# Optimization experiments

Hardware: AMD Instinct MI355X
Metric: run time of the kernel (lower is better)

The kernel has to match this reference:

```python
import jax, jax.numpy as jnp
import numpy as np

N = 50000
E = 800000
NEG_SLOPE = 0.2  # PyG GATConv default


def gat_conv(x, src, dst, W, att_src, att_dst, bias, heads, out_ch, concat):
    # x: [N, F_in]; W: [F_in, heads*out_ch]; att_*: [heads, out_ch]; bias: [heads*out_ch] or [out_ch]
    h = (x @ W).reshape(N, heads, out_ch)                       # [N, H, C]
    a_src = jnp.sum(h * att_src, axis=-1)                       # [N, H]
    a_dst = jnp.sum(h * att_dst, axis=-1)                       # [N, H]
    e = jax.nn.leaky_relu(a_src[src] + a_dst[dst], NEG_SLOPE)   # [E', H]
    # numerically stable scatter-softmax over incoming edges of each dst node
    e_max = jax.ops.segment_max(e, dst, num_segments=N)         # [N, H]
    ex = jnp.exp(e - e_max[dst])                                # [E', H]
    denom = jax.ops.segment_sum(ex, dst, num_segments=N)        # [N, H]
    alpha = ex / denom[dst]                                     # [E', H]
    msg = h[src] * alpha[:, :, None]                            # [E', H, C]
    out = jax.ops.segment_sum(msg, dst, num_segments=N)         # [N, H, C]
    out = out.reshape(N, heads * out_ch) if concat else out.mean(axis=1)
    return out + bias


def setup_inputs() -> dict:
    key = jax.random.key(0)
    ks = jax.random.split(key, 16)
    s = 0.05
    x = jax.random.normal(ks[0], (N, 128), dtype=jnp.float32)
    edge_index = jax.random.randint(ks[1], (2, E), 0, N, dtype=jnp.int64)
    H, C = 8, 64
    return {
        "x": x,
        "edge_index": edge_index,
        "W0": jax.random.normal(ks[2], (128, H * C), dtype=jnp.float32) * s,
        "as0": jax.random.normal(ks[3], (H, C), dtype=jnp.float32) * s,
        "ad0": jax.random.normal(ks[4], (H, C), dtype=jnp.float32) * s,
        "b0": jnp.zeros((H * C,), dtype=jnp.float32),
        "W1": jax.random.normal(ks[5], (H * C, H * C), dtype=jnp.float32) * s,
        "as1": jax.random.normal(ks[6], (H, C), dtype=jnp.float32) * s,
        "ad1": jax.random.normal(ks[7], (H, C), dtype=jnp.float32) * s,
        "b1": jnp.zeros((H * C,), dtype=jnp.float32),
        "W2": jax.random.normal(ks[8], (H * C, 40), dtype=jnp.float32) * s,
        "as2": jax.random.normal(ks[9], (1, 40), dtype=jnp.float32) * s,
        "ad2": jax.random.normal(ks[10], (1, 40), dtype=jnp.float32) * s,
        "b2": jnp.zeros((40,), dtype=jnp.float32),
    }


def reference(x, edge_index, W0, as0, ad0, b0, W1, as1, ad1, b1, W2, as2, ad2, b2):
    # add self-loops (PyG GATConv default add_self_loops=True)
    loop = jnp.arange(N, dtype=edge_index.dtype)
    src = jnp.concatenate([edge_index[0], loop])
    dst = jnp.concatenate([edge_index[1], loop])
    h = gat_conv(x, src, dst, W0, as0, ad0, b0, heads=8, out_ch=64, concat=True)
    h = jax.nn.relu(h)  # dropout is identity at inference
    h = gat_conv(h, src, dst, W1, as1, ad1, b1, heads=8, out_ch=64, concat=True)
    h = jax.nn.relu(h)
    h = gat_conv(h, src, dst, W2, as2, ad2, b2, heads=1, out_ch=40, concat=False)
    return jax.nn.log_softmax(h, axis=1)
```

## Files before the change

### kernel.cpp

```cpp
#include <hip/hip_runtime.h>
#include <hip/hip_bf16.h>
#include <hip/hip_fp16.h>
#include <math.h>

#define N_NODES 50000
#define N_EDGES 800000
#define TOT_EDGES (N_EDGES + N_NODES)
#define NEG_SLOPE 0.2f
#define M_PAD 50048
#define N_CHUNKS ((N_NODES + 1023) / 1024)

typedef __attribute__((ext_vector_type(8))) short bf16x8;
typedef __attribute__((ext_vector_type(4))) float f32x4;
typedef __attribute__((ext_vector_type(8))) unsigned short u16x8;

__device__ __forceinline__ unsigned short f2bf(float f){
  union { float f; unsigned u; } x; x.f = f;
  unsigned r = x.u + 0x7FFF + ((x.u >> 16) & 1);
  return (unsigned short)(r >> 16);
}
__device__ __forceinline__ float bf2f(unsigned short h){
  union { unsigned u; float f; } x; x.u = ((unsigned)h) << 16;
  return x.f;
}
__device__ __forceinline__ void gl_lds16(const void* g, void* l){
  __builtin_amdgcn_global_load_lds(
    (const __attribute__((address_space(1))) unsigned int*)g,
    (__attribute__((address_space(3))) unsigned int*)l, 16, 0, 0);
}


__global__ void hist_kernel(const int* __restrict__ ei, int* __restrict__ counts){
  int e = blockIdx.x*256 + threadIdx.x;
  if (e >= TOT_EDGES) return;
  int d = (e < N_EDGES) ? ei[N_EDGES + e] : (e - N_EDGES);
  atomicAdd(&counts[d], 1);
}

__global__ void scan1_kernel(const int* __restrict__ counts, int* __restrict__ partial,
                             int* __restrict__ chunksum){
  __shared__ int sm[1024];
  int t = threadIdx.x;
  int idx = blockIdx.x*1024 + t;
  int v = (idx < N_NODES) ? counts[idx] : 0;
  sm[t] = v;
  __syncthreads();
  for (int off = 1; off < 1024; off <<= 1){
    int u = (t >= off) ? sm[t-off] : 0;
    __syncthreads();
    sm[t] += u;
    __syncthreads();
  }
  if (idx < N_NODES) partial[idx] = sm[t];
  if (t == 1023) chunksum[blockIdx.x] = sm[1023];
}

__global__ void scan2_kernel(const int* __restrict__ chunksum, int* __restrict__ carry){
  if (threadIdx.x == 0){
    int c = 0;
    for (int i = 0; i < N_CHUNKS; ++i){ carry[i] = c; c += chunksum[i]; }
  }
}

__global__ void scan3_kernel(const int* __restrict__ partial, const int* __restrict__ counts,
                             const int* __restrict__ carry, int* __restrict__ offsets,
                             int* __restrict__ cursor){
  int idx = blockIdx.x*256 + threadIdx.x;
  if (idx >= N_NODES) return;
  int inc = partial[idx] + carry[idx >> 10];
  offsets[idx+1] = inc;
  cursor[idx] = inc - counts[idx];
  if (idx == 0) offsets[0] = 0;
}

__global__ void scatter_kernel(const int* __restrict__ ei, int* __restrict__ cursor,
                               int* __restrict__ ssrc){
  int e = blockIdx.x*256 + threadIdx.x;
  if (e >= TOT_EDGES) return;
  int s, d;
  if (e < N_EDGES){ s = ei[e]; d = ei[N_EDGES+e]; } else { s = e - N_EDGES; d = s; }
  int pos = atomicAdd(&cursor[d], 1);
  ssrc[pos] = s;
}


__global__ void convert_BT(const float* __restrict__ B, unsigned short* __restrict__ BTh,
                           unsigned short* __restrict__ BTl, int K, int N){
  int id = blockIdx.x*256 + threadIdx.x;
  if (id >= K*N) return;
  int n = id / K, k = id - n*K;
  float v = B[(size_t)k*N + n];
  unsigned short h = f2bf(v);
  unsigned short l = f2bf(v - bf2f(h));
  BTh[id] = h; BTl[id] = l;
}

__global__ void convert_BT2(const float* __restrict__ B, unsigned short* __restrict__ BTh,
                            unsigned short* __restrict__ BTl){
  int id = blockIdx.x*256 + threadIdx.x;
  if (id >= 128*512) return;
  int n = id >> 9, k = id & 511;
  float v = (n < 40) ? B[(size_t)k*40 + n] : 0.f;
  unsigned short h = f2bf(v);
  unsigned short l = f2bf(v - bf2f(h));
  BTh[id] = h; BTl[id] = l;
}

__global__ void split_x(const float* __restrict__ X, unsigned short* __restrict__ Xh,
                        unsigned short* __restrict__ Xl){
  int id = blockIdx.x*256 + threadIdx.x;
  if (id >= M_PAD*128) return;
  int row = id >> 7;
  float v = (row < N_NODES) ? X[(size_t)row*128 + (id & 127)] : 0.f;
  unsigned short h = f2bf(v);
  unsigned short l = f2bf(v - bf2f(h));
  Xh[id] = h; Xl[id] = l;
}


__global__ __launch_bounds__(256, 2) void mfma_gemm(
    const unsigned short* __restrict__ Ah_g, const unsigned short* __restrict__ Al_g,
    const unsigned short* __restrict__ BTh, const unsigned short* __restrict__ BTl,
    float* __restrict__ C, unsigned short* __restrict__ FbS,
    const float* __restrict__ att_s, const float* __restrict__ att_d,
    float* __restrict__ asrc, float* __restrict__ adst,
    int M, int K, int Nc)
{
  __shared__ unsigned short sAh[128*32];
  __shared__ unsigned short sAl[128*32];
  __shared__ unsigned short sBh[128*32];
  __shared__ unsigned short sBl[128*32];

  const int tid = threadIdx.x;
  const int lane = tid & 63;
  const int wid = tid >> 6;
  const int wr = wid >> 1, wc = wid & 1;
  const int bm = blockIdx.y * 128, bn = blockIdx.x * 128;
  const int lr = lane & 15, kg = lane >> 4;

  size_t agoff[2], bgoff[2];
  #pragma unroll
  for (int i = 0; i < 2; ++i){
    int o = tid + i*256;
    int row = o >> 2, ch = o & 3;
    int sc = ch ^ ((row >> 1) & 3);
    agoff[i] = (size_t)(bm + row)*K + sc*8;
    bgoff[i] = (size_t)(bn + row)*K + sc*8;
  }
  int aoff[4], boff[4];
  #pragma unroll
  for (int i = 0; i < 4; ++i){
    int row = wr*64 + i*16 + lr;
    aoff[i] = row*32 + (kg ^ ((row >> 1) & 3))*8;
    int col = wc*64 + i*16 + lr;
    boff[i] = col*32 + (kg ^ ((col >> 1) & 3))*8;
  }

  auto stage = [&](int k0){
    #pragma unroll
    for (int i = 0; i < 2; ++i){
      gl_lds16(Ah_g + agoff[i] + k0, &sAh[(tid + i*256)*8]);
      gl_lds16(Al_g + agoff[i] + k0, &sAl[(tid + i*256)*8]);
      gl_lds16(BTh + bgoff[i] + k0, &sBh[(tid + i*256)*8]);
      gl_lds16(BTl + bgoff[i] + k0, &sBl[(tid + i*256)*8]);
    }
  };

  f32x4 acc[4][4];
  #pragma unroll
  for (int i = 0; i < 4; ++i)
    #pragma unroll
    for (int j = 0; j < 4; ++j)
      acc[i][j] = (f32x4){0.f, 0.f, 0.f, 0.f};

  stage(0);
  __syncthreads();
  int k0 = 0;
  while (true){
    bf16x8 ah[4], al[4], bh[4], bl[4];
    #pragma unroll
    for (int i = 0; i < 4; ++i){
      ah[i] = *(const bf16x8*)&sAh[aoff[i]];
      al[i] = *(const bf16x8*)&sAl[aoff[i]];
      bh[i] = *(const bf16x8*)&sBh[boff[i]];
      bl[i] = *(const bf16x8*)&sBl[boff[i]];
    }
    #pragma unroll
    for (int i = 0; i < 4; ++i)
      #pragma unroll
      for (int j = 0; j < 4; ++j){
        acc[i][j] = __builtin_amdgcn_mfma_f32_16x16x32_bf16(ah[i], bh[j], acc[i][j], 0, 0, 0);
        acc[i][j] = __builtin_amdgcn_mfma_f32_16x16x32_bf16(al[i], bh[j], acc[i][j], 0, 0, 0);
        acc[i][j] = __builtin_amdgcn_mfma_f32_16x16x32_bf16(ah[i], bl[j], acc[i][j], 0, 0, 0);
      }
    int kn = k0 + 32;
    if (kn >= K) break;
    __syncthreads();
    stage(kn);
    __syncthreads();
    k0 = kn;
  }

  if (att_s){
    int head = (bn >> 6) + wc;
    float ws_[4], wd_[4];
    #pragma unroll
    for (int j = 0; j < 4; ++j){
      ws_[j] = att_s[head*64 + j*16 + lr];
      wd_[j] = att_d[head*64 + j*16 + lr];
    }
    #pragma unroll
    for (int i = 0; i < 4; ++i){
      #pragma unroll
      for (int r = 0; r < 4; ++r){
        float vs = 0.f, vd = 0.f;
        #pragma unroll
        for (int j = 0; j < 4; ++j){
          vs += acc[i][j][r] * ws_[j];
          vd += acc[i][j][r] * wd_[j];
        }
        #pragma unroll
        for (int m = 1; m < 16; m <<= 1){
          vs += __shfl_xor(vs, m);
          vd += __shfl_xor(vd, m);
        }
        int gm = bm + wr*64 + i*16 + kg*4 + r;
        if ((lane & 15) == 0 && gm < M){
          asrc[gm*8 + head] = vs;
          adst[gm*8 + head] = vd;
        }
      }
    }
  }

  #pragma unroll
  for (int i = 0; i < 4; ++i){
    int gm0 = bm + wr*64 + i*16 + kg*4;
    #pragma unroll
    for (int j = 0; j < 4; ++j){
      int gn = bn + wc*64 + j*16 + lr;
      int sl = gn >> 5, cc = gn & 31;
      #pragma unroll
      for (int r = 0; r < 4; ++r){
        int gm = gm0 + r;
        if (gm < M){
          if (C && gn < Nc) C[(size_t)gm*Nc + gn] = acc[i][j][r];
          if (FbS) FbS[(size_t)sl*(M_PAD*32) + (size_t)gm*32 + cc] = f2bf(acc[i][j][r]);
        }
      }
    }
  }
}


__global__ __launch_bounds__(256) void softmax_stats(const int* __restrict__ offsets,
    const int* __restrict__ ssrc, const float* __restrict__ asrc,
    const float* __restrict__ adst, unsigned* __restrict__ EA){
  int w = threadIdx.x >> 6;
  int lane = threadIdx.x & 63;
  int d = blockIdx.x*4 + w;
  if (d >= N_NODES) return;
  int h = lane & 7, grp = lane >> 3;
  int beg = offsets[d], end = offsets[d+1];
  float ad = adst[d*8+h];
  float pm = -1e30f;
  for (int i = beg+grp; i < end; i += 8){
    int s = ssrc[i];
    float e = asrc[s*8+h] + ad;
    e = (e > 0.f) ? e : NEG_SLOPE*e;
    pm = fmaxf(pm, e);
  }
  pm = fmaxf(pm, __shfl_xor(pm, 8));
  pm = fmaxf(pm, __shfl_xor(pm, 16));
  pm = fmaxf(pm, __shfl_xor(pm, 32));
  float ps = 0.f;
  for (int i = beg+grp; i < end; i += 8){
    int s = ssrc[i];
    float e = asrc[s*8+h] + ad;
    e = (e > 0.f) ? e : NEG_SLOPE*e;
    ps += __expf(e - pm);
  }
  ps += __shfl_xor(ps, 8);
  ps += __shfl_xor(ps, 16);
  ps += __shfl_xor(ps, 32);
  float iv = 1.f / ps;
  unsigned* Eh = EA + (size_t)h * TOT_EDGES;
  for (int i = beg+grp; i < end; i += 8){
    int s = ssrc[i];
    float e = asrc[s*8+h] + ad;
    e = (e > 0.f) ? e : NEG_SLOPE*e;
    float al = __expf(e - pm) * iv;
    union { __half hh; unsigned short u; } cv; cv.hh = __float2half(al);
    unsigned pk = (unsigned)s | ((unsigned)cv.u << 16);
    __builtin_nontemporal_store(pk, &Eh[i]);
  }
}


__global__ __launch_bounds__(256) void spmm_kernel(const unsigned short* __restrict__ FbS,
    const int* __restrict__ offsets, const unsigned* __restrict__ EA,
    const float* __restrict__ bias, unsigned short* __restrict__ Fh,
    unsigned short* __restrict__ Fl, int do_relu){
  __shared__ unsigned sEA[1024];
  int bid = blockIdx.x;
  int half = (bid >= 25000) ? 1 : 0;
  int r = bid - half*25000;
  int slice = (r & 7) + half*8;
  int chunk = r >> 3;
  int lane = threadIdx.x & 63;
  int wid = threadIdx.x >> 6;
  int dsub = lane >> 4;
  int slot = (lane >> 2) & 3;
  int ch = lane & 3;
  int dbase = chunk*16;
  int d = dbase + wid*4 + dsub;
  int h = slice >> 1;
  const unsigned short* Ft = FbS + (size_t)slice * (M_PAD*32);
  const unsigned* Eh = EA + (size_t)h * TOT_EDGES;
  int beg0 = offsets[dbase];
  int cnt = min(offsets[dbase+16] - beg0, 1024);
  for (int i = threadIdx.x; i < cnt; i += 256)
    sEA[i] = __builtin_nontemporal_load(&Eh[beg0 + i]);
  __syncthreads();
  int beg = offsets[d], end = offsets[d+1];
  float a0=0.f,a1=0.f,a2=0.f,a3=0.f,a4=0.f,a5=0.f,a6=0.f,a7=0.f;
  #pragma unroll 2
  for (int i = beg + slot; i < end; i += 4){
    int idx = i - beg0;
    unsigned ea = (idx < cnt) ? sEA[idx] : __builtin_nontemporal_load(&Eh[i]);
    int s = ea & 0xFFFF;
    union { unsigned short u; __half hh; } dv; dv.u = (unsigned short)(ea >> 16);
    float al = __half2float(dv.hh);
    uint4 v = *(const uint4*)&Ft[(size_t)s*32 + ch*8];
    union { unsigned q; float f; } lo, hi;
    lo.q = v.x << 16; hi.q = v.x & 0xffff0000u; a0 += al*lo.f; a1 += al*hi.f;
    lo.q = v.y << 16; hi.q = v.y & 0xffff0000u; a2 += al*lo.f; a3 += al*hi.f;
    lo.q = v.z << 16; hi.q = v.z & 0xffff0000u; a4 += al*lo.f; a5 += al*hi.f;
    lo.q = v.w << 16; hi.q = v.w & 0xffff0000u; a6 += al*lo.f; a7 += al*hi.f;
  }
  a0 += __shfl_xor(a0, 4); a0 += __shfl_xor(a0, 8);
  a1 += __shfl_xor(a1, 4); a1 += __shfl_xor(a1, 8);
  a2 += __shfl_xor(a2, 4); a2 += __shfl_xor(a2, 8);
  a3 += __shfl_xor(a3, 4); a3 += __shfl_xor(a3, 8);
  a4 += __shfl_xor(a4, 4); a4 += __shfl_xor(a4, 8);
  a5 += __shfl_xor(a5, 4); a5 += __shfl_xor(a5, 8);
  a6 += __shfl_xor(a6, 4); a6 += __shfl_xor(a6, 8);
  a7 += __shfl_xor(a7, 4); a7 += __shfl_xor(a7, 8);
  if (slot == 0){
    int c = slice*32 + ch*8;
    float4 b0v = *(const float4*)&bias[c];
    float4 b1v = *(const float4*)&bias[c+4];
    float oo[8];
    oo[0]=a0+b0v.x; oo[1]=a1+b0v.y; oo[2]=a2+b0v.z; oo[3]=a3+b0v.w;
    oo[4]=a4+b1v.x; oo[5]=a5+b1v.y; oo[6]=a6+b1v.z; oo[7]=a7+b1v.w;
    u16x8 vh, vl;
    #pragma unroll
    for (int q = 0; q < 8; ++q){
      float v = oo[q];
      if (do_relu) v = fmaxf(v, 0.f);
      unsigned short hb = f2bf(v);
      vh[q] = hb;
      vl[q] = f2bf(v - bf2f(hb));
    }
    size_t base = (size_t)d*512 + c;
    *(u16x8*)&Fh[base] = vh;
    *(u16x8*)&Fl[base] = vl;
  }
}


__global__ void attn_coef2_kernel(const float* __restrict__ H2v, const float* __restrict__ as2,
                                  const float* __restrict__ ad2,
                                  float* __restrict__ asrc, float* __restrict__ adst){
  int gid = blockIdx.x*256 + threadIdx.x;
  int node = gid >> 6;
  int lane = threadIdx.x & 63;
  if (node >= N_NODES) return;
  float v = 0.f, ws = 0.f, wd = 0.f;
  if (lane < 40){ v = H2v[(size_t)node*40 + lane]; ws = as2[lane]; wd = ad2[lane]; }
  float vs = v*ws, vd = v*wd;
  #pragma unroll
  for (int off = 32; off > 0; off >>= 1){
    vs += __shfl_down(vs, off);
    vd += __shfl_down(vd, off);
  }
  if (lane == 0){ asrc[node] = vs; adst[node] = vd; }
}

__global__ __launch_bounds__(64) void aggregate2_kernel(const float* __restrict__ H2v,
    const int* __restrict__ offsets, const int* __restrict__ ssrc,
    const float* __restrict__ asrc, const float* __restrict__ adst,
    const float* __restrict__ bias, float* __restrict__ OUT){
  int d = blockIdx.x;
  int lane = threadIdx.x;
  int beg = offsets[d], end = offsets[d+1];
  int deg = end - beg;
  float ad = adst[d];
  float pm = -1e30f;
  for (int i = lane; i < deg; i += 64){
    int s = ssrc[beg+i];
    float e = asrc[s] + ad; e = (e>0.f)?e:NEG_SLOPE*e;
    pm = fmaxf(pm, e);
  }
  #pragma unroll
  for (int off = 32; off > 0; off >>= 1) pm = fmaxf(pm, __shfl_xor(pm, off));
  float ps = 0.f;
  for (int i = lane; i < deg; i += 64){
    int s = ssrc[beg+i];
    float e = asrc[s] + ad; e=(e>0.f)?e:NEG_SLOPE*e;
    ps += __expf(e - pm);
  }
  #pragma unroll
  for (int off = 32; off > 0; off >>= 1) ps += __shfl_xor(ps, off);
  float inv = 1.f/ps;
  __shared__ float alS[64];
  __shared__ int sS[64];
  float acc = 0.f;
  for (int i0 = 0; i0 < deg; i0 += 64){
    int nch = min(64, deg - i0);
    if (lane < nch){
      int s = ssrc[beg+i0+lane];
      float e = asrc[s]+ad; e=(e>0.f)?e:NEG_SLOPE*e;
      alS[lane] = __expf(e-pm)*inv;
      sS[lane] = s;
    }
    __syncthreads();
    for (int i = 0; i < nch; ++i){
      if (lane < 40) acc += alS[i] * H2v[(size_t)sS[i]*40 + lane];
    }
    __syncthreads();
  }
  float logit = (lane<40) ? (acc + bias[lane]) : -1e30f;
  float mm = logit;
  #pragma unroll
  for (int off = 32; off > 0; off >>= 1) mm = fmaxf(mm, __shfl_xor(mm, off));
  float ex = (lane<40) ? __expf(logit-mm) : 0.f;
  float ss = ex;
  #pragma unroll
  for (int off = 32; off > 0; off >>= 1) ss += __shfl_xor(ss, off);
  if (lane < 40) OUT[(size_t)d*40 + lane] = logit - mm - logf(ss);
}


extern "C" void kernel_launch(void* const* d_in, const int* in_sizes, int n_in,
                              void* d_out, int out_size, void* d_ws, size_t ws_size,
                              hipStream_t stream){
  const float* x   = (const float*)d_in[0];
  const int*   ei  = (const int*)d_in[1];
  const float* W0  = (const float*)d_in[2];
  const float* as0 = (const float*)d_in[3];
  const float* ad0 = (const float*)d_in[4];
  const float* b0  = (const float*)d_in[5];
  const float* W1  = (const float*)d_in[6];
  const float* as1 = (const float*)d_in[7];
  const float* ad1 = (const float*)d_in[8];
  const float* b1  = (const float*)d_in[9];
  const float* W2  = (const float*)d_in[10];
  const float* as2 = (const float*)d_in[11];
  const float* ad2 = (const float*)d_in[12];
  const float* b2  = (const float*)d_in[13];
  float* out = (float*)d_out;

  char* p = (char*)d_ws;
  auto alloc = [&](size_t bytes)->void*{
    void* r = (void*)p; p += (bytes + 255) & ~(size_t)255; return r;
  };
  unsigned short* F1h = (unsigned short*)alloc((size_t)M_PAD*512*2);
  unsigned short* F1l = (unsigned short*)alloc((size_t)M_PAD*512*2);
  unsigned short* FbS = (unsigned short*)alloc((size_t)M_PAD*512*2);
  unsigned short* Xh  = (unsigned short*)alloc((size_t)M_PAD*128*2);
  unsigned short* Xl  = (unsigned short*)alloc((size_t)M_PAD*128*2);
  float* ASRC  = (float*)alloc((size_t)N_NODES*8*4);
  float* ADST  = (float*)alloc((size_t)N_NODES*8*4);
  unsigned* EA = (unsigned*)alloc((size_t)8*TOT_EDGES*4);
  float* H2v   = (float*)alloc((size_t)N_NODES*40*4);
  float* ASRC2 = (float*)alloc((size_t)N_NODES*4);
  float* ADST2 = (float*)alloc((size_t)N_NODES*4);
  int* counts  = (int*)alloc((size_t)N_NODES*4);
  int* offsets = (int*)alloc((size_t)(N_NODES+1)*4);
  int* cursor  = (int*)alloc((size_t)N_NODES*4);
  int* ssrc    = (int*)alloc((size_t)TOT_EDGES*4);
  int* partial = (int*)alloc((size_t)N_NODES*4);
  int* chunksum= (int*)alloc(64*4);
  int* carry   = (int*)alloc(64*4);
  unsigned short* BTh  = (unsigned short*)alloc((size_t)512*512*2);
  unsigned short* BTl  = (unsigned short*)alloc((size_t)512*512*2);
  unsigned short* BT2h = (unsigned short*)alloc((size_t)128*512*2);
  unsigned short* BT2l = (unsigned short*)alloc((size_t)128*512*2);

  hipMemsetAsync(F1h + (size_t)N_NODES*512, 0, (size_t)(M_PAD-N_NODES)*512*2, stream);
  hipMemsetAsync(F1l + (size_t)N_NODES*512, 0, (size_t)(M_PAD-N_NODES)*512*2, stream);

  hipMemsetAsync(counts, 0, (size_t)N_NODES*4, stream);
  hist_kernel<<<(TOT_EDGES+255)/256, 256, 0, stream>>>(ei, counts);
  scan1_kernel<<<N_CHUNKS, 1024, 0, stream>>>(counts, partial, chunksum);
  scan2_kernel<<<1, 64, 0, stream>>>(chunksum, carry);
  scan3_kernel<<<(N_NODES+255)/256, 256, 0, stream>>>(partial, counts, carry, offsets, cursor);
  scatter_kernel<<<(TOT_EDGES+255)/256, 256, 0, stream>>>(ei, cursor, ssrc);

  int mt = M_PAD / 128;
  int spmm_blocks = 2 * 8 * 3125;

  split_x<<<(M_PAD*128+255)/256, 256, 0, stream>>>(x, Xh, Xl);
  convert_BT<<<(128*512+255)/256, 256, 0, stream>>>(W0, BTh, BTl, 128, 512);
  mfma_gemm<<<dim3(4, mt), 256, 0, stream>>>(Xh, Xl, BTh, BTl, nullptr, FbS,
                                             as0, ad0, ASRC, ADST, N_NODES, 128, 512);
  softmax_stats<<<(N_NODES+3)/4, 256, 0, stream>>>(offsets, ssrc, ASRC, ADST, EA);
  spmm_kernel<<<spmm_blocks, 256, 0, stream>>>(FbS, offsets, EA, b0, F1h, F1l, 1);

  convert_BT<<<(512*512+255)/256, 256, 0, stream>>>(W1, BTh, BTl, 512, 512);
  mfma_gemm<<<dim3(4, mt), 256, 0, stream>>>(F1h, F1l, BTh, BTl, nullptr, FbS,
                                             as1, ad1, ASRC, ADST, N_NODES, 512, 512);
  softmax_stats<<<(N_NODES+3)/4, 256, 0, stream>>>(offsets, ssrc, ASRC, ADST, EA);
  spmm_kernel<<<spmm_blocks, 256, 0, stream>>>(FbS, offsets, EA, b1, F1h, F1l, 1);

  convert_BT2<<<(128*512+255)/256, 256, 0, stream>>>(W2, BT2h, BT2l);
  mfma_gemm<<<dim3(1, mt), 256, 0, stream>>>(F1h, F1l, BT2h, BT2l, H2v, nullptr,
                                             nullptr, nullptr, nullptr, nullptr, N_NODES, 512, 40);
  attn_coef2_kernel<<<(N_NODES*64+255)/256, 256, 0, stream>>>(H2v, as2, ad2, ASRC2, ADST2);
  aggregate2_kernel<<<N_NODES, 64, 0, stream>>>(H2v, offsets, ssrc, ASRC2, ADST2, b2, out);
}
```

Baseline: 767.6 us.

## Switch GEMM to fp16 two-term split, online softmax stats, drop spmm LDS staging

The split-bf16 GEMM becomes fp16 MFMA. A is still split into high and low halves, but B is a single fp16 copy, so each tile needs two MFMAs instead of three and one fewer LDS buffer. The softmax stats kernel now computes max and sum in one online pass instead of two passes over the edges. The spmm kernel drops its LDS prefetch of edge data and loads it directly, and features are stored as fp16 rather than bf16. fp16 has a narrower range than bf16 and B loses its low-order correction, which risks accuracy or overflow.

```diff
diff --git a/kernel.cpp b/kernel.cpp
--- a/kernel.cpp
+++ b/kernel.cpp
@@ -10,18 +10,15 @@
 #define M_PAD 50048
 #define N_CHUNKS ((N_NODES + 1023) / 1024)
 
-typedef __attribute__((ext_vector_type(8))) short bf16x8;
+typedef __attribute__((ext_vector_type(8))) _Float16 f16x8;
 typedef __attribute__((ext_vector_type(4))) float f32x4;
 typedef __attribute__((ext_vector_type(8))) unsigned short u16x8;
 
-__device__ __forceinline__ unsigned short f2bf(float f){
-  union { float f; unsigned u; } x; x.f = f;
-  unsigned r = x.u + 0x7FFF + ((x.u >> 16) & 1);
-  return (unsigned short)(r >> 16);
-}
-__device__ __forceinline__ float bf2f(unsigned short h){
-  union { unsigned u; float f; } x; x.u = ((unsigned)h) << 16;
-  return x.f;
+__device__ __forceinline__ unsigned short f2h(float f){
+  union { _Float16 h; unsigned short u; } c; c.h = (_Float16)f; return c.u;
+}
+__device__ __forceinline__ float h2f(unsigned short u){
+  union { unsigned short u; _Float16 h; } c; c.u = u; return (float)c.h;
 }
 __device__ __forceinline__ void gl_lds16(const void* g, void* l){
   __builtin_amdgcn_global_load_lds(
@@ -84,26 +81,19 @@
 }
 
 
-__global__ void convert_BT(const float* __restrict__ B, unsigned short* __restrict__ BTh,
-                           unsigned short* __restrict__ BTl, int K, int N){
+__global__ void convert_BT(const float* __restrict__ B, unsigned short* __restrict__ BT,
+                           int K, int N){
   int id = blockIdx.x*256 + threadIdx.x;
   if (id >= K*N) return;
   int n = id / K, k = id - n*K;
-  float v = B[(size_t)k*N + n];
-  unsigned short h = f2bf(v);
-  unsigned short l = f2bf(v - bf2f(h));
-  BTh[id] = h; BTl[id] = l;
-}
-
-__global__ void convert_BT2(const float* __restrict__ B, unsigned short* __restrict__ BTh,
-                            unsigned short* __restrict__ BTl){
+  BT[id] = f2h(B[(size_t)k*N + n]);
+}
+
+__global__ void convert_BT2(const float* __restrict__ B, unsigned short* __restrict__ BT){
   int id = blockIdx.x*256 + threadIdx.x;
   if (id >= 128*512) return;
   int n = id >> 9, k = id & 511;
-  float v = (n < 40) ? B[(size_t)k*40 + n] : 0.f;
-  unsigned short h = f2bf(v);
-  unsigned short l = f2bf(v - bf2f(h));
-  BTh[id] = h; BTl[id] = l;
+  BT[id] = f2h((n < 40) ? B[(size_t)k*40 + n] : 0.f);
 }
 
 __global__ void split_x(const float* __restrict__ X, unsigned short* __restrict__ Xh,
@@ -112,15 +102,15 @@
   if (id >= M_PAD*128) return;
   int row = id >> 7;
   float v = (row < N_NODES) ? X[(size_t)row*128 + (id & 127)] : 0.f;
-  unsigned short h = f2bf(v);
-  unsigned short l = f2bf(v - bf2f(h));
-  Xh[id] = h; Xl[id] = l;
+  unsigned short h = f2h(v);
+  Xh[id] = h;
+  Xl[id] = f2h(v - h2f(h));
 }
 
 
 __global__ __launch_bounds__(256, 2) void mfma_gemm(
     const unsigned short* __restrict__ Ah_g, const unsigned short* __restrict__ Al_g,
-    const unsigned short* __restrict__ BTh, const unsigned short* __restrict__ BTl,
+    const unsigned short* __restrict__ BT,
     float* __restrict__ C, unsigned short* __restrict__ FbS,
     const float* __restrict__ att_s, const float* __restrict__ att_d,
     float* __restrict__ asrc, float* __restrict__ adst,
@@ -128,8 +118,7 @@
 {
   __shared__ unsigned short sAh[128*32];
   __shared__ unsigned short sAl[128*32];
-  __shared__ unsigned short sBh[128*32];
-  __shared__ unsigned short sBl[128*32];
+  __shared__ unsigned short sB[128*32];
 
   const int tid = threadIdx.x;
   const int lane = tid & 63;
@@ -161,8 +150,7 @@
     for (int i = 0; i < 2; ++i){
       gl_lds16(Ah_g + agoff[i] + k0, &sAh[(tid + i*256)*8]);
       gl_lds16(Al_g + agoff[i] + k0, &sAl[(tid + i*256)*8]);
-      gl_lds16(BTh + bgoff[i] + k0, &sBh[(tid + i*256)*8]);
-      gl_lds16(BTl + bgoff[i] + k0, &sBl[(tid + i*256)*8]);
+      gl_lds16(BT + bgoff[i] + k0, &sB[(tid + i*256)*8]);
     }
   };
 
@@ -177,21 +165,19 @@
   __syncthreads();
   int k0 = 0;
   while (true){
-    bf16x8 ah[4], al[4], bh[4], bl[4];
+    f16x8 ah[4], al[4], b[4];
     #pragma unroll
     for (int i = 0; i < 4; ++i){
-      ah[i] = *(const bf16x8*)&sAh[aoff[i]];
-      al[i] = *(const bf16x8*)&sAl[aoff[i]];
-      bh[i] = *(const bf16x8*)&sBh[boff[i]];
-      bl[i] = *(const bf16x8*)&sBl[boff[i]];
+      ah[i] = *(const f16x8*)&sAh[aoff[i]];
+      al[i] = *(const f16x8*)&sAl[aoff[i]];
+      b[i]  = *(const f16x8*)&sB[boff[i]];
     }
     #pragma unroll
     for (int i = 0; i < 4; ++i)
       #pragma unroll
       for (int j = 0; j < 4; ++j){
-        acc[i][j] = __builtin_amdgcn_mfma_f32_16x16x32_bf16(ah[i], bh[j], acc[i][j], 0, 0, 0);
-        acc[i][j] = __builtin_amdgcn_mfma_f32_16x16x32_bf16(al[i], bh[j], acc[i][j], 0, 0, 0);
-        acc[i][j] = __builtin_amdgcn_mfma_f32_16x16x32_bf16(ah[i], bl[j], acc[i][j], 0, 0, 0);
+        acc[i][j] = __builtin_amdgcn_mfma_f32_16x16x32_f16(ah[i], b[j], acc[i][j], 0, 0, 0);
+        acc[i][j] = __builtin_amdgcn_mfma_f32_16x16x32_f16(al[i], b[j], acc[i][j], 0, 0, 0);
       }
     int kn = k0 + 32;
     if (kn >= K) break;
@@ -245,7 +231,7 @@
         int gm = gm0 + r;
         if (gm < M){
           if (C && gn < Nc) C[(size_t)gm*Nc + gn] = acc[i][j][r];
-          if (FbS) FbS[(size_t)sl*(M_PAD*32) + (size_t)gm*32 + cc] = f2bf(acc[i][j][r]);
+          if (FbS) FbS[(size_t)sl*(M_PAD*32) + (size_t)gm*32 + cc] = f2h(acc[i][j][r]);
         }
       }
     }
@@ -263,35 +249,30 @@
   int h = lane & 7, grp = lane >> 3;
   int beg = offsets[d], end = offsets[d+1];
   float ad = adst[d*8+h];
-  float pm = -1e30f;
+  float m = -1e30f, s = 0.f;
   for (int i = beg+grp; i < end; i += 8){
-    int s = ssrc[i];
-    float e = asrc[s*8+h] + ad;
+    int sv = ssrc[i];
+    float e = asrc[sv*8+h] + ad;
     e = (e > 0.f) ? e : NEG_SLOPE*e;
-    pm = fmaxf(pm, e);
-  }
-  pm = fmaxf(pm, __shfl_xor(pm, 8));
-  pm = fmaxf(pm, __shfl_xor(pm, 16));
-  pm = fmaxf(pm, __shfl_xor(pm, 32));
-  float ps = 0.f;
-  for (int i = beg+grp; i < end; i += 8){
-    int s = ssrc[i];
-    float e = asrc[s*8+h] + ad;
-    e = (e > 0.f) ? e : NEG_SLOPE*e;
-    ps += __expf(e - pm);
-  }
-  ps += __shfl_xor(ps, 8);
-  ps += __shfl_xor(ps, 16);
-  ps += __shfl_xor(ps, 32);
-  float iv = 1.f / ps;
+    if (e > m){ s = s*__expf(m - e) + 1.f; m = e; }
+    else s += __expf(e - m);
+  }
+  #pragma unroll
+  for (int k = 8; k < 64; k <<= 1){
+    float mo = __shfl_xor(m, k);
+    float so = __shfl_xor(s, k);
+    float M = fmaxf(m, mo);
+    s = s*__expf(m - M) + so*__expf(mo - M);
+    m = M;
+  }
+  float iv = 1.f / s;
   unsigned* Eh = EA + (size_t)h * TOT_EDGES;
   for (int i = beg+grp; i < end; i += 8){
-    int s = ssrc[i];
-    float e = asrc[s*8+h] + ad;
+    int sv = ssrc[i];
+    float e = asrc[sv*8+h] + ad;
     e = (e > 0.f) ? e : NEG_SLOPE*e;
-    float al = __expf(e - pm) * iv;
-    union { __half hh; unsigned short u; } cv; cv.hh = __float2half(al);
-    unsigned pk = (unsigned)s | ((unsigned)cv.u << 16);
+    float al = __expf(e - m) * iv;
+    unsigned pk = (unsigned)sv | ((unsigned)f2h(al) << 16);
     __builtin_nontemporal_store(pk, &Eh[i]);
   }
 }
@@ -301,7 +282,6 @@
     const int* __restrict__ offsets, const unsigned* __restrict__ EA,
     const float* __restrict__ bias, unsigned short* __restrict__ Fh,
     unsigned short* __restrict__ Fl, int do_relu){
-  __shared__ unsigned sEA[1024];
   int bid = blockIdx.x;
   int half = (bid >= 25000) ? 1 : 0;
   int r = bid - half*25000;
@@ -312,31 +292,27 @@
   int dsub = lane >> 4;
   int slot = (lane >> 2) & 3;
   int ch = lane & 3;
-  int dbase = chunk*16;
-  int d = dbase + wid*4 + dsub;
+  int d = chunk*16 + wid*4 + dsub;
   int h = slice >> 1;
   const unsigned short* Ft = FbS + (size_t)slice * (M_PAD*32);
   const unsigned* Eh = EA + (size_t)h * TOT_EDGES;
-  int beg0 = offsets[dbase];
-  int cnt = min(offsets[dbase+16] - beg0, 1024);
-  for (int i = threadIdx.x; i < cnt; i += 256)
-    sEA[i] = __builtin_nontemporal_load(&Eh[beg0 + i]);
-  __syncthreads();
-  int beg = offsets[d], end = offsets[d+1];
+  int2 oo = *(const int2*)&offsets[d];
+  int beg = oo.x, end = oo.y;
   float a0=0.f,a1=0.f,a2=0.f,a3=0.f,a4=0.f,a5=0.f,a6=0.f,a7=0.f;
   #pragma unroll 2
   for (int i = beg + slot; i < end; i += 4){
-    int idx = i - beg0;
-    unsigned ea = (idx < cnt) ? sEA[idx] : __builtin_nontemporal_load(&Eh[i]);
+    unsigned ea = __builtin_nontemporal_load(&Eh[i]);
     int s = ea & 0xFFFF;
-    union { unsigned short u; __half hh; } dv; dv.u = (unsigned short)(ea >> 16);
-    float al = __half2float(dv.hh);
-    uint4 v = *(const uint4*)&Ft[(size_t)s*32 + ch*8];
-    union { unsigned q; float f; } lo, hi;
-    lo.q = v.x << 16; hi.q = v.x & 0xffff0000u; a0 += al*lo.f; a1 += al*hi.f;
-    lo.q = v.y << 16; hi.q = v.y & 0xffff0000u; a2 += al*lo.f; a3 += al*hi.f;
-    lo.q = v.z << 16; hi.q = v.z & 0xffff0000u; a4 += al*lo.f; a5 += al*hi.f;
-    lo.q = v.w << 16; hi.q = v.w & 0xffff0000u; a6 += al*lo.f; a7 += al*hi.f;
+    float al = h2f((unsigned short)(ea >> 16));
+    f16x8 v = *(const f16x8*)&Ft[(size_t)s*32 + ch*8];
+    a0 += al * (float)v[0];
+    a1 += al * (float)v[1];
+    a2 += al * (float)v[2];
+    a3 += al * (float)v[3];
+    a4 += al * (float)v[4];
+    a5 += al * (float)v[5];
+    a6 += al * (float)v[6];
+    a7 += al * (float)v[7];
   }
   a0 += __shfl_xor(a0, 4); a0 += __shfl_xor(a0, 8);
   a1 += __shfl_xor(a1, 4); a1 += __shfl_xor(a1, 8);
@@ -350,17 +326,17 @@
     int c = slice*32 + ch*8;
     float4 b0v = *(const float4*)&bias[c];
     float4 b1v = *(const float4*)&bias[c+4];
-    float oo[8];
-    oo[0]=a0+b0v.x; oo[1]=a1+b0v.y; oo[2]=a2+b0v.z; oo[3]=a3+b0v.w;
-    oo[4]=a4+b1v.x; oo[5]=a5+b1v.y; oo[6]=a6+b1v.z; oo[7]=a7+b1v.w;
+    float oo_[8];
+    oo_[0]=a0+b0v.x; oo_[1]=a1+b0v.y; oo_[2]=a2+b0v.z; oo_[3]=a3+b0v.w;
+    oo_[4]=a4+b1v.x; oo_[5]=a5+b1v.y; oo_[6]=a6+b1v.z; oo_[7]=a7+b1v.w;
     u16x8 vh, vl;
     #pragma unroll
     for (int q = 0; q < 8; ++q){
-      float v = oo[q];
+      float v = oo_[q];
       if (do_relu) v = fmaxf(v, 0.f);
-      unsigned short hb = f2bf(v);
+      unsigned short hb = f2h(v);
       vh[q] = hb;
-      vl[q] = f2bf(v - bf2f(hb));
+      vl[q] = f2h(v - h2f(hb));
     }
     size_t base = (size_t)d*512 + c;
     *(u16x8*)&Fh[base] = vh;
@@ -483,10 +459,8 @@
   int* partial = (int*)alloc((size_t)N_NODES*4);
   int* chunksum= (int*)alloc(64*4);
   int* carry   = (int*)alloc(64*4);
-  unsigned short* BTh  = (unsigned short*)alloc((size_t)512*512*2);
-  unsigned short* BTl  = (unsigned short*)alloc((size_t)512*512*2);
-  unsigned short* BT2h = (unsigned short*)alloc((size_t)128*512*2);
-  unsigned short* BT2l = (unsigned short*)alloc((size_t)128*512*2);
+  unsigned short* BT  = (unsigned short*)alloc((size_t)512*512*2);
+  unsigned short* BT2 = (unsigned short*)alloc((size_t)128*512*2);
 
   hipMemsetAsync(F1h + (size_t)N_NODES*512, 0, (size_t)(M_PAD-N_NODES)*512*2, stream);
   hipMemsetAsync(F1l + (size_t)N_NODES*512, 0, (size_t)(M_PAD-N_NODES)*512*2, stream);
@@ -502,20 +476,20 @@
   int spmm_blocks = 2 * 8 * 3125;
 
   split_x<<<(M_PAD*128+255)/256, 256, 0, stream>>>(x, Xh, Xl);
-  convert_BT<<<(128*512+255)/256, 256, 0, stream>>>(W0, BTh, BTl, 128, 512);
-  mfma_gemm<<<dim3(4, mt), 256, 0, stream>>>(Xh, Xl, BTh, BTl, nullptr, FbS,
+  convert_BT<<<(128*512+255)/256, 256, 0, stream>>>(W0, BT, 128, 512);
+  mfma_gemm<<<dim3(4, mt), 256, 0, stream>>>(Xh, Xl, BT, nullptr, FbS,
                                              as0, ad0, ASRC, ADST, N_NODES, 128, 512);
   softmax_stats<<<(N_NODES+3)/4, 256, 0, stream>>>(offsets, ssrc, ASRC, ADST, EA);
   spmm_kernel<<<spmm_blocks, 256, 0, stream>>>(FbS, offsets, EA, b0, F1h, F1l, 1);
 
-  convert_BT<<<(512*512+255)/256, 256, 0, stream>>>(W1, BTh, BTl, 512, 512);
-  mfma_gemm<<<dim3(4, mt), 256, 0, stream>>>(F1h, F1l, BTh, BTl, nullptr, FbS,
+  convert_BT<<<(512*512+255)/256, 256, 0, stream>>>(W1, BT, 512, 512);
+  mfma_gemm<<<dim3(4, mt), 256, 0, stream>>>(F1h, F1l, BT, nullptr, FbS,
                                              as1, ad1, ASRC, ADST, N_NODES, 512, 512);
   softmax_stats<<<(N_NODES+3)/4, 256, 0, stream>>>(offsets, ssrc, ASRC, ADST, EA);
   spmm_kernel<<<spmm_blocks, 256, 0, stream>>>(FbS, offsets, EA, b1, F1h, F1l, 1);
 
-  convert_BT2<<<(128*512+255)/256, 256, 0, stream>>>(W2, BT2h, BT2l);
-  mfma_gemm<<<dim3(1, mt), 256, 0, stream>>>(F1h, F1l, BT2h, BT2l, H2v, nullptr,
+  convert_BT2<<<(128*512+255)/256, 256, 0, stream>>>(W2, BT2);
+  mfma_gemm<<<dim3(1, mt), 256, 0, stream>>>(F1h, F1l, BT2, H2v, nullptr,
                                              nullptr, nullptr, nullptr, nullptr, N_NODES, 512, 40);
   attn_coef2_kernel<<<(N_NODES*64+255)/256, 256, 0, stream>>>(H2v, as2, ad2, ASRC2, ADST2);
   aggregate2_kernel<<<N_NODES, 64, 0, stream>>>(H2v, offsets, ssrc, ASRC2, ADST2, b2, out);
```

Measured after the change: 808.7 us. 5.4% more time.
